# Performance work log

Hardware: AMD Instinct MI355X
Metric: run time of the kernel (lower is better)

Reference implementation:

```python
import jax, jax.numpy as jnp
import numpy as np

B, N, E, IN_DIM, OUT_DIM = 8, 4500, 72000, 128, 128
EPS = 1e-5  # torch LayerNorm default


def setup_inputs() -> dict:
    key = jax.random.key(0)
    k0, k1, k2 = jax.random.split(key, 3)
    node_features = jax.random.normal(k0, (B, N, IN_DIM), dtype=jnp.float32)
    edge_index = jax.random.randint(k1, (B, 2, E), 0, N, dtype=jnp.int64)
    node_mask = jnp.ones((B, N), dtype=jnp.float32)
    edge_mask = jnp.ones((B, E), dtype=jnp.float32)
    W = (jax.random.normal(k2, (OUT_DIM, IN_DIM), dtype=jnp.float32)
         / np.float32(np.sqrt(IN_DIM)))
    b = jnp.zeros((OUT_DIM,), dtype=jnp.float32)
    gamma = jnp.ones((OUT_DIM,), dtype=jnp.float32)
    beta = jnp.zeros((OUT_DIM,), dtype=jnp.float32)
    return {"node_features": node_features, "edge_index": edge_index,
            "node_mask": node_mask, "edge_mask": edge_mask,
            "W": W, "b": b, "gamma": gamma, "beta": beta}


def reference(node_features, edge_index, node_mask, edge_mask, W, b, gamma, beta):
    Bsz, Nn, _ = node_features.shape
    # linear transform: h = x W^T + b  -> [B, N, out_dim]
    h = jnp.einsum('bni,oi->bno', node_features, W) + b
    D = h.shape[-1]
    total = Bsz * Nn

    # With all nodes valid, the sparse index of node (b, n) is b*Nn + n.
    offsets = (jnp.arange(Bsz, dtype=edge_index.dtype) * Nn)[:, None]  # [B,1]
    src = (edge_index[:, 0, :] + offsets).reshape(-1)  # [B*E]
    tgt = (edge_index[:, 1, :] + offsets).reshape(-1)  # [B*E]
    ew = edge_mask.reshape(-1)                          # [B*E] edge validity

    flat_h = h.reshape(total, D)

    # in-degree (valid edges only) + self-loop, D^{-1/2} normalization
    deg = jax.ops.segment_sum(ew, tgt, num_segments=total) + 1.0
    dinv = deg ** -0.5

    coef = dinv[src] * dinv[tgt] * ew                   # [B*E]
    msg = flat_h[src] * coef[:, None]                   # gather + weight
    agg = jax.ops.segment_sum(msg, tgt, num_segments=total)
    agg = agg + flat_h * dinv[:, None]                  # self contribution

    h = h + agg.reshape(Bsz, Nn, D)                     # residual

    # dropout is identity at inference; LayerNorm then ReLU then mask
    mu = jnp.mean(h, axis=-1, keepdims=True)
    var = jnp.mean((h - mu) ** 2, axis=-1, keepdims=True)
    h = (h - mu) / jnp.sqrt(var + EPS) * gamma + beta
    h = jax.nn.relu(h) * node_mask[..., None]
    return h
```

## Files before the change

kernel.cpp:

```cpp
#include <hip/hip_runtime.h>
#include <math.h>

typedef unsigned short ushort_t;
typedef unsigned int uint_t;
typedef __attribute__((ext_vector_type(8))) short bf16x8;
typedef __attribute__((ext_vector_type(16))) float f32x16;

constexpr int Bc   = 8;
constexpr int Nn   = 4500;
constexpr int Ec   = 72000;
constexpr int D    = 128;
constexpr int T    = Bc * Nn;
constexpr int TE   = Bc * Ec;
constexpr float EPS = 1e-5f;

constexpr int PAD = 32;
constexpr int RST = 64;

constexpr int NB_W    = 64;
constexpr int NB_Z    = (T * PAD / 4) / 256;
constexpr int NB_PREP = NB_W + NB_Z;

constexpr int NB_ECH  = (Ec + 255) / 256;
constexpr int NB_EDGE = 8 * NB_ECH;

constexpr int NB_GEMM = ((T / 32) * 2 + 3) / 4;

constexpr size_t WS_CNTP  = 0;
constexpr size_t WS_EDATA = 4608000;
constexpr size_t WS_DINV  = 13824000;
constexpr size_t WS_WHI   = 13968000;
constexpr size_t WS_WLO   = 14000768;
constexpr size_t WS_H     = 14033536;

__device__ __forceinline__ ushort_t f32_to_bf16_rne(float f) {
  uint_t u = __float_as_uint(f);
  uint_t r = (u + 0x7fffu + ((u >> 16) & 1u)) >> 16;
  return (ushort_t)r;
}
__device__ __forceinline__ float bf16_to_f32(ushort_t h) {
  return __uint_as_float(((uint_t)h) << 16);
}

__global__ __launch_bounds__(256) void prep_kernel(
    const float* __restrict__ W, ushort_t* __restrict__ Whi,
    ushort_t* __restrict__ Wlo, int4* __restrict__ cntp4) {
  const int bid = blockIdx.x;
  if (bid < NB_W) {
    int i = bid * 256 + threadIdx.x;
    float w = W[i];
    ushort_t hi = f32_to_bf16_rne(w);
    Whi[i] = hi;
    Wlo[i] = f32_to_bf16_rne(w - bf16_to_f32(hi));
  } else {
    int i = (bid - NB_W) * 256 + threadIdx.x;
    cntp4[i] = make_int4(0, 0, 0, 0);
  }
}

__global__ __launch_bounds__(256) void edge_kernel(
    const int* __restrict__ ei, const float* __restrict__ em,
    int* __restrict__ cntp, uint_t* __restrict__ edata) {
  const int b  = blockIdx.x & 7;
  const int el = (blockIdx.x >> 3) * 256 + threadIdx.x;
  if (el >= Ec) return;
  const int* eb = ei + b * 2 * Ec;
  int t0 = eb[Ec + el];
  if ((unsigned)t0 >= (unsigned)Nn) return;
  int tg = t0 + b * Nn;
  int rk = atomicAdd(&cntp[(size_t)tg * PAD], 1);
  if (rk >= RST) return;
  int s0 = eb[el];
  float ew = em[b * Ec + el];
  uint_t sl = (uint_t)s0;
  if ((unsigned)s0 >= (unsigned)Nn) { sl = 0; ew = 0.f; }
  uint_t pk = ((uint_t)f32_to_bf16_rne(ew) << 16) | sl;
  edata[(size_t)tg * RST + rk] = pk;
}

__global__ __launch_bounds__(256) void dinv_kernel(
    const uint_t* __restrict__ edata, const int* __restrict__ cntp,
    float* __restrict__ dinv) {
  int i = blockIdx.x * 256 + threadIdx.x;
  if (i >= T) return;
  int cnt = cntp[(size_t)i * PAD];
  cnt = (cnt > RST) ? RST : cnt;
  const uint_t* row = edata + (size_t)i * RST;
  float s = 0.f;
  for (int j = 0; j < cnt; ++j) s += bf16_to_f32((ushort_t)(row[j] >> 16));
  dinv[i] = 1.0f / sqrtf(s + 1.0f);
}

__global__ __launch_bounds__(256) void gemm_kernel(
    const float* __restrict__ x, const ushort_t* __restrict__ Whi,
    const ushort_t* __restrict__ Wlo, const float* __restrict__ bias,
    float* __restrict__ h) {
  const int g = blockIdx.x * 4 + (threadIdx.x >> 6);
  if (g >= (T / 32) * 2) return;
  const int lane = threadIdx.x & 63;
  const int mt = g >> 1;
  const int nh = g & 1;
  const int m0 = mt * 32;
  const int r  = lane & 31;
  const int kh = lane >> 5;

  const float* xrow = x + (size_t)(m0 + r) * D + kh * 8;

  f32x16 acc[2];
#pragma unroll
  for (int n = 0; n < 2; ++n)
#pragma unroll
    for (int j = 0; j < 16; ++j) acc[n][j] = 0.f;

#pragma unroll
  for (int ks = 0; ks < 8; ++ks) {
    const float4 p0 = ((const float4*)(xrow + ks * 16))[0];
    const float4 p1 = ((const float4*)(xrow + ks * 16))[1];
    const float xa[8] = {p0.x, p0.y, p0.z, p0.w, p1.x, p1.y, p1.z, p1.w};
    bf16x8 ahi, alo;
#pragma unroll
    for (int j = 0; j < 8; ++j) {
      ushort_t hb = f32_to_bf16_rne(xa[j]);
      ahi[j] = (short)hb;
      alo[j] = (short)f32_to_bf16_rne(xa[j] - bf16_to_f32(hb));
    }
#pragma unroll
    for (int n = 0; n < 2; ++n) {
      const size_t boff = (size_t)((nh * 2 + n) * 32 + r) * D + ks * 16 + kh * 8;
      bf16x8 bhi = *(const bf16x8*)(Whi + boff);
      bf16x8 blo = *(const bf16x8*)(Wlo + boff);
      acc[n] = __builtin_amdgcn_mfma_f32_32x32x16_bf16(ahi, bhi, acc[n], 0, 0, 0);
      acc[n] = __builtin_amdgcn_mfma_f32_32x32x16_bf16(ahi, blo, acc[n], 0, 0, 0);
      acc[n] = __builtin_amdgcn_mfma_f32_32x32x16_bf16(alo, bhi, acc[n], 0, 0, 0);
    }
  }

#pragma unroll
  for (int n = 0; n < 2; ++n) {
    const int col = (nh * 2 + n) * 32 + r;
    const float bv = bias[col];
#pragma unroll
    for (int j = 0; j < 16; ++j) {
      const int mrow = m0 + (j & 3) + 8 * (j >> 2) + 4 * kh;
      h[(size_t)mrow * D + col] = acc[n][j] + bv;
    }
  }
}

__global__ __launch_bounds__(256) void gather_ln_kernel(
    const float* __restrict__ h, const int* __restrict__ cntp,
    const uint_t* __restrict__ edata, const float* __restrict__ dinv,
    const float* __restrict__ gamma, const float* __restrict__ beta,
    const float* __restrict__ mask, float* __restrict__ out) {
  const int bid  = blockIdx.x;
  const int b    = bid & 7;
  const int wid  = threadIdx.x >> 6;
  const int node = b * Nn + (bid >> 3) * 4 + wid;
  const int bOff = b * Nn;
  const int lane = threadIdx.x & 63;
  const int f4   = lane & 31;
  const int half = lane >> 5;

  const float4* h4 = (const float4*)h;
  int cnt = cntp[(size_t)node * PAD];
  cnt = (cnt > RST) ? RST : cnt;
  const uint_t* row = edata + (size_t)node * RST;

  float4 hv = h4[(size_t)node * 32 + f4];

  float4 accE = make_float4(0.f, 0.f, 0.f, 0.f);
  int i = half;
  for (; i + 6 < cnt; i += 8) {
    uint_t p0 = row[i];
    uint_t p1 = row[i + 2];
    uint_t p2 = row[i + 4];
    uint_t p3 = row[i + 6];
    int sg0 = bOff + (p0 & 0xFFFFu);
    int sg1 = bOff + (p1 & 0xFFFFu);
    int sg2 = bOff + (p2 & 0xFFFFu);
    int sg3 = bOff + (p3 & 0xFFFFu);
    float c0 = dinv[sg0] * bf16_to_f32((ushort_t)(p0 >> 16));
    float c1 = dinv[sg1] * bf16_to_f32((ushort_t)(p1 >> 16));
    float c2 = dinv[sg2] * bf16_to_f32((ushort_t)(p2 >> 16));
    float c3 = dinv[sg3] * bf16_to_f32((ushort_t)(p3 >> 16));
    float4 v0 = h4[(size_t)sg0 * 32 + f4];
    float4 v1 = h4[(size_t)sg1 * 32 + f4];
    float4 v2 = h4[(size_t)sg2 * 32 + f4];
    float4 v3 = h4[(size_t)sg3 * 32 + f4];
    accE.x += v0.x * c0 + v1.x * c1 + v2.x * c2 + v3.x * c3;
    accE.y += v0.y * c0 + v1.y * c1 + v2.y * c2 + v3.y * c3;
    accE.z += v0.z * c0 + v1.z * c1 + v2.z * c2 + v3.z * c3;
    accE.w += v0.w * c0 + v1.w * c1 + v2.w * c2 + v3.w * c3;
  }
  for (; i < cnt; i += 2) {
    uint_t p0 = row[i];
    int sg0 = bOff + (p0 & 0xFFFFu);
    float c0 = dinv[sg0] * bf16_to_f32((ushort_t)(p0 >> 16));
    float4 v0 = h4[(size_t)sg0 * 32 + f4];
    accE.x += v0.x * c0;
    accE.y += v0.y * c0;
    accE.z += v0.z * c0;
    accE.w += v0.w * c0;
  }

  accE.x += __shfl_xor(accE.x, 32);
  accE.y += __shfl_xor(accE.y, 32);
  accE.z += __shfl_xor(accE.z, 32);
  accE.w += __shfl_xor(accE.w, 32);

  const float dt = dinv[node];
  float4 acc;
  acc.x = hv.x * (1.f + dt) + dt * accE.x;
  acc.y = hv.y * (1.f + dt) + dt * accE.y;
  acc.z = hv.z * (1.f + dt) + dt * accE.z;
  acc.w = hv.w * (1.f + dt) + dt * accE.w;

  float su = acc.x + acc.y + acc.z + acc.w;
  float ss = acc.x * acc.x + acc.y * acc.y + acc.z * acc.z + acc.w * acc.w;
#pragma unroll
  for (int o = 16; o > 0; o >>= 1) {
    su += __shfl_xor(su, o);
    ss += __shfl_xor(ss, o);
  }
  float mu  = su * (1.0f / 128.0f);
  float var = ss * (1.0f / 128.0f) - mu * mu;
  float rs  = 1.0f / sqrtf(var + EPS);
  float m   = mask[node];

  float4 g  = ((const float4*)gamma)[f4];
  float4 bb = ((const float4*)beta)[f4];
  float4 rv;
  rv.x = fmaxf((acc.x - mu) * rs * g.x + bb.x, 0.f) * m;
  rv.y = fmaxf((acc.y - mu) * rs * g.y + bb.y, 0.f) * m;
  rv.z = fmaxf((acc.z - mu) * rs * g.z + bb.z, 0.f) * m;
  rv.w = fmaxf((acc.w - mu) * rs * g.w + bb.w, 0.f) * m;
  if (half == 0) ((float4*)out)[(size_t)node * 32 + f4] = rv;
}

extern "C" void kernel_launch(void* const* d_in, const int* in_sizes, int n_in,
                              void* d_out, int out_size, void* d_ws, size_t ws_size,
                              hipStream_t stream) {
  const float* x     = (const float*)d_in[0];
  const int*   ei    = (const int*)d_in[1];
  const float* nmask = (const float*)d_in[2];
  const float* emask = (const float*)d_in[3];
  const float* W     = (const float*)d_in[4];
  const float* bias  = (const float*)d_in[5];
  const float* gamma = (const float*)d_in[6];
  const float* beta  = (const float*)d_in[7];
  float* out = (float*)d_out;

  char*     ws    = (char*)d_ws;
  int*      cntp  = (int*)     (ws + WS_CNTP);
  uint_t*   edata = (uint_t*)  (ws + WS_EDATA);
  float*    dinv  = (float*)   (ws + WS_DINV);
  ushort_t* Whi   = (ushort_t*)(ws + WS_WHI);
  ushort_t* Wlo   = (ushort_t*)(ws + WS_WLO);
  float*    h     = (float*)   (ws + WS_H);

  prep_kernel<<<NB_PREP, 256, 0, stream>>>(W, Whi, Wlo, (int4*)cntp);
  edge_kernel<<<NB_EDGE, 256, 0, stream>>>(ei, emask, cntp, edata);
  dinv_kernel<<<(T + 255) / 256, 256, 0, stream>>>(edata, cntp, dinv);
  gemm_kernel<<<NB_GEMM, 256, 0, stream>>>(x, Whi, Wlo, bias, h);
  gather_ln_kernel<<<T / 4, 256, 0, stream>>>(h, cntp, edata, dinv,
                                              gamma, beta, nmask, out);
}
```

Before: 87.53 us.

## Store h in bf16 and merge dinv computation into GEMM launch

```diff
diff --git a/kernel.cpp b/kernel.cpp
--- a/kernel.cpp
+++ b/kernel.cpp
@@ -25,6 +25,8 @@
 constexpr int NB_EDGE = 8 * NB_ECH;
 
 constexpr int NB_GEMM = ((T / 32) * 2 + 3) / 4;
+constexpr int NB_DINV = 8 * 18;
+constexpr int NB_GD   = NB_GEMM + NB_DINV;
 
 constexpr size_t WS_CNTP  = 0;
 constexpr size_t WS_EDATA = 4608000;
@@ -78,77 +80,80 @@
   edata[(size_t)tg * RST + rk] = pk;
 }
 
-__global__ __launch_bounds__(256) void dinv_kernel(
-    const uint_t* __restrict__ edata, const int* __restrict__ cntp,
-    float* __restrict__ dinv) {
-  int i = blockIdx.x * 256 + threadIdx.x;
-  if (i >= T) return;
-  int cnt = cntp[(size_t)i * PAD];
-  cnt = (cnt > RST) ? RST : cnt;
-  const uint_t* row = edata + (size_t)i * RST;
-  float s = 0.f;
-  for (int j = 0; j < cnt; ++j) s += bf16_to_f32((ushort_t)(row[j] >> 16));
-  dinv[i] = 1.0f / sqrtf(s + 1.0f);
-}
-
-__global__ __launch_bounds__(256) void gemm_kernel(
+__global__ __launch_bounds__(256) void gemm_dinv_kernel(
     const float* __restrict__ x, const ushort_t* __restrict__ Whi,
     const ushort_t* __restrict__ Wlo, const float* __restrict__ bias,
-    float* __restrict__ h) {
-  const int g = blockIdx.x * 4 + (threadIdx.x >> 6);
-  if (g >= (T / 32) * 2) return;
-  const int lane = threadIdx.x & 63;
-  const int mt = g >> 1;
-  const int nh = g & 1;
-  const int m0 = mt * 32;
-  const int r  = lane & 31;
-  const int kh = lane >> 5;
-
-  const float* xrow = x + (size_t)(m0 + r) * D + kh * 8;
-
-  f32x16 acc[2];
-#pragma unroll
-  for (int n = 0; n < 2; ++n)
-#pragma unroll
-    for (int j = 0; j < 16; ++j) acc[n][j] = 0.f;
-
-#pragma unroll
-  for (int ks = 0; ks < 8; ++ks) {
-    const float4 p0 = ((const float4*)(xrow + ks * 16))[0];
-    const float4 p1 = ((const float4*)(xrow + ks * 16))[1];
-    const float xa[8] = {p0.x, p0.y, p0.z, p0.w, p1.x, p1.y, p1.z, p1.w};
-    bf16x8 ahi, alo;
-#pragma unroll
-    for (int j = 0; j < 8; ++j) {
-      ushort_t hb = f32_to_bf16_rne(xa[j]);
-      ahi[j] = (short)hb;
-      alo[j] = (short)f32_to_bf16_rne(xa[j] - bf16_to_f32(hb));
+    ushort_t* __restrict__ h, const uint_t* __restrict__ edata,
+    const int* __restrict__ cntp, float* __restrict__ dinv) {
+  const int bid = blockIdx.x;
+  if (bid < NB_GEMM) {
+    const int g = bid * 4 + (threadIdx.x >> 6);
+    if (g >= (T / 32) * 2) return;
+    const int lane = threadIdx.x & 63;
+    const int mt = g >> 1;
+    const int nh = g & 1;
+    const int m0 = mt * 32;
+    const int r  = lane & 31;
+    const int kh = lane >> 5;
+
+    const float* xrow = x + (size_t)(m0 + r) * D + kh * 8;
+
+    f32x16 acc[2];
+#pragma unroll
+    for (int n = 0; n < 2; ++n)
+#pragma unroll
+      for (int j = 0; j < 16; ++j) acc[n][j] = 0.f;
+
+#pragma unroll
+    for (int ks = 0; ks < 8; ++ks) {
+      const float4 p0 = ((const float4*)(xrow + ks * 16))[0];
+      const float4 p1 = ((const float4*)(xrow + ks * 16))[1];
+      const float xa[8] = {p0.x, p0.y, p0.z, p0.w, p1.x, p1.y, p1.z, p1.w};
+      bf16x8 ahi, alo;
+#pragma unroll
+      for (int j = 0; j < 8; ++j) {
+        ushort_t hb = f32_to_bf16_rne(xa[j]);
+        ahi[j] = (short)hb;
+        alo[j] = (short)f32_to_bf16_rne(xa[j] - bf16_to_f32(hb));
+      }
+#pragma unroll
+      for (int n = 0; n < 2; ++n) {
+        const size_t boff = (size_t)((nh * 2 + n) * 32 + r) * D + ks * 16 + kh * 8;
+        bf16x8 bhi = *(const bf16x8*)(Whi + boff);
+        bf16x8 blo = *(const bf16x8*)(Wlo + boff);
+        acc[n] = __builtin_amdgcn_mfma_f32_32x32x16_bf16(ahi, bhi, acc[n], 0, 0, 0);
+        acc[n] = __builtin_amdgcn_mfma_f32_32x32x16_bf16(ahi, blo, acc[n], 0, 0, 0);
+        acc[n] = __builtin_amdgcn_mfma_f32_32x32x16_bf16(alo, bhi, acc[n], 0, 0, 0);
+      }
     }
+
 #pragma unroll
     for (int n = 0; n < 2; ++n) {
-      const size_t boff = (size_t)((nh * 2 + n) * 32 + r) * D + ks * 16 + kh * 8;
-      bf16x8 bhi = *(const bf16x8*)(Whi + boff);
-      bf16x8 blo = *(const bf16x8*)(Wlo + boff);
-      acc[n] = __builtin_amdgcn_mfma_f32_32x32x16_bf16(ahi, bhi, acc[n], 0, 0, 0);
-      acc[n] = __builtin_amdgcn_mfma_f32_32x32x16_bf16(ahi, blo, acc[n], 0, 0, 0);
-      acc[n] = __builtin_amdgcn_mfma_f32_32x32x16_bf16(alo, bhi, acc[n], 0, 0, 0);
+      const int col = (nh * 2 + n) * 32 + r;
+      const float bv = bias[col];
+#pragma unroll
+      for (int j = 0; j < 16; ++j) {
+        const int mrow = m0 + (j & 3) + 8 * (j >> 2) + 4 * kh;
+        h[(size_t)mrow * D + col] = f32_to_bf16_rne(acc[n][j] + bv);
+      }
     }
-  }
-
-#pragma unroll
-  for (int n = 0; n < 2; ++n) {
-    const int col = (nh * 2 + n) * 32 + r;
-    const float bv = bias[col];
-#pragma unroll
-    for (int j = 0; j < 16; ++j) {
-      const int mrow = m0 + (j & 3) + 8 * (j >> 2) + 4 * kh;
-      h[(size_t)mrow * D + col] = acc[n][j] + bv;
-    }
+  } else {
+    const int zb = bid - NB_GEMM;
+    const int b  = zb & 7;
+    const int nl = (zb >> 3) * 256 + threadIdx.x;
+    if (nl >= Nn) return;
+    const int i = b * Nn + nl;
+    int cnt = cntp[(size_t)i * PAD];
+    cnt = (cnt > RST) ? RST : cnt;
+    const uint_t* row = edata + (size_t)i * RST;
+    float s = 0.f;
+    for (int j = 0; j < cnt; ++j) s += bf16_to_f32((ushort_t)(row[j] >> 16));
+    dinv[i] = 1.0f / sqrtf(s + 1.0f);
   }
 }
 
 __global__ __launch_bounds__(256) void gather_ln_kernel(
-    const float* __restrict__ h, const int* __restrict__ cntp,
+    const ushort_t* __restrict__ h, const int* __restrict__ cntp,
     const uint_t* __restrict__ edata, const float* __restrict__ dinv,
     const float* __restrict__ gamma, const float* __restrict__ beta,
     const float* __restrict__ mask, float* __restrict__ out) {
@@ -161,12 +166,14 @@
   const int f4   = lane & 31;
   const int half = lane >> 5;
 
-  const float4* h4 = (const float4*)h;
+  const ushort4* h4 = (const ushort4*)h;
   int cnt = cntp[(size_t)node * PAD];
   cnt = (cnt > RST) ? RST : cnt;
   const uint_t* row = edata + (size_t)node * RST;
 
-  float4 hv = h4[(size_t)node * 32 + f4];
+  ushort4 hq = h4[(size_t)node * 32 + f4];
+  float4 hv = make_float4(bf16_to_f32(hq.x), bf16_to_f32(hq.y),
+                          bf16_to_f32(hq.z), bf16_to_f32(hq.w));
 
   float4 accE = make_float4(0.f, 0.f, 0.f, 0.f);
   int i = half;
@@ -183,24 +190,28 @@
     float c1 = dinv[sg1] * bf16_to_f32((ushort_t)(p1 >> 16));
     float c2 = dinv[sg2] * bf16_to_f32((ushort_t)(p2 >> 16));
     float c3 = dinv[sg3] * bf16_to_f32((ushort_t)(p3 >> 16));
-    float4 v0 = h4[(size_t)sg0 * 32 + f4];
-    float4 v1 = h4[(size_t)sg1 * 32 + f4];
-    float4 v2 = h4[(size_t)sg2 * 32 + f4];
-    float4 v3 = h4[(size_t)sg3 * 32 + f4];
-    accE.x += v0.x * c0 + v1.x * c1 + v2.x * c2 + v3.x * c3;
-    accE.y += v0.y * c0 + v1.y * c1 + v2.y * c2 + v3.y * c3;
-    accE.z += v0.z * c0 + v1.z * c1 + v2.z * c2 + v3.z * c3;
-    accE.w += v0.w * c0 + v1.w * c1 + v2.w * c2 + v3.w * c3;
+    ushort4 q0 = h4[(size_t)sg0 * 32 + f4];
+    ushort4 q1 = h4[(size_t)sg1 * 32 + f4];
+    ushort4 q2 = h4[(size_t)sg2 * 32 + f4];
+    ushort4 q3 = h4[(size_t)sg3 * 32 + f4];
+    accE.x += bf16_to_f32(q0.x) * c0 + bf16_to_f32(q1.x) * c1 +
+              bf16_to_f32(q2.x) * c2 + bf16_to_f32(q3.x) * c3;
+    accE.y += bf16_to_f32(q0.y) * c0 + bf16_to_f32(q1.y) * c1 +
+              bf16_to_f32(q2.y) * c2 + bf16_to_f32(q3.y) * c3;
+    accE.z += bf16_to_f32(q0.z) * c0 + bf16_to_f32(q1.z) * c1 +
+              bf16_to_f32(q2.z) * c2 + bf16_to_f32(q3.z) * c3;
+    accE.w += bf16_to_f32(q0.w) * c0 + bf16_to_f32(q1.w) * c1 +
+              bf16_to_f32(q2.w) * c2 + bf16_to_f32(q3.w) * c3;
   }
   for (; i < cnt; i += 2) {
     uint_t p0 = row[i];
     int sg0 = bOff + (p0 & 0xFFFFu);
     float c0 = dinv[sg0] * bf16_to_f32((ushort_t)(p0 >> 16));
-    float4 v0 = h4[(size_t)sg0 * 32 + f4];
-    accE.x += v0.x * c0;
-    accE.y += v0.y * c0;
-    accE.z += v0.z * c0;
-    accE.w += v0.w * c0;
+    ushort4 q0 = h4[(size_t)sg0 * 32 + f4];
+    accE.x += bf16_to_f32(q0.x) * c0;
+    accE.y += bf16_to_f32(q0.y) * c0;
+    accE.z += bf16_to_f32(q0.z) * c0;
+    accE.w += bf16_to_f32(q0.w) * c0;
   }
 
   accE.x += __shfl_xor(accE.x, 32);
@@ -256,12 +267,12 @@
   float*    dinv  = (float*)   (ws + WS_DINV);
   ushort_t* Whi   = (ushort_t*)(ws + WS_WHI);
   ushort_t* Wlo   = (ushort_t*)(ws + WS_WLO);
-  float*    h     = (float*)   (ws + WS_H);
+  ushort_t* h     = (ushort_t*)(ws + WS_H);
 
   prep_kernel<<<NB_PREP, 256, 0, stream>>>(W, Whi, Wlo, (int4*)cntp);
   edge_kernel<<<NB_EDGE, 256, 0, stream>>>(ei, emask, cntp, edata);
-  dinv_kernel<<<(T + 255) / 256, 256, 0, stream>>>(edata, cntp, dinv);
-  gemm_kernel<<<NB_GEMM, 256, 0, stream>>>(x, Whi, Wlo, bias, h);
+  gemm_dinv_kernel<<<NB_GD, 256, 0, stream>>>(x, Whi, Wlo, bias, h,
+                                              edata, cntp, dinv);
   gather_ln_kernel<<<T / 4, 256, 0, stream>>>(h, cntp, edata, dinv,
                                               gamma, beta, nmask, out);
 }
```

Result: faster. 81.22 us (-7.2%).
